# Kernel optimization log

Hardware: AMD Instinct MI355X
Metric: run time of the kernel (lower is better)

Reference implementation:

```python
import jax, jax.numpy as jnp
import numpy as np

B, N, K, Q = 2, 4096, 48, 20  # batch, nodes, neighbors, Potts states (amino acids)


def setup_inputs() -> dict:
    key = jax.random.key(0)
    k1, k2, k3, k4 = jax.random.split(key, 4)
    h = jax.random.normal(k1, (B, N, Q), dtype=jnp.float32)
    J = jax.random.normal(k2, (B, N, K, Q, Q), dtype=jnp.float32)
    edge_idx = jax.random.randint(k3, (B, N, K), 0, N)
    S = jax.random.randint(k4, (B, N), 0, Q)
    return {"S": S, "h": h, "J": J, "edge_idx": edge_idx}


def reference(S, h, J, edge_idx):
    """Potts energy: U (B,), U_i (B,N,Q). Faithful to compute_potts_energy."""
    Bs, Ns, Ks, Qs, _ = J.shape
    # collect_neighbors: S_j[b,i,k] = S[b, edge_idx[b,i,k]]
    S_j = jnp.take_along_axis(S, edge_idx.reshape(Bs, Ns * Ks), axis=1).reshape(Bs, Ns, Ks)
    # J_ij[b,i,k,q] = J[b,i,k,q, S_j[b,i,k]]  (gather along last state axis)
    idx = jnp.broadcast_to(S_j[..., None, None], (Bs, Ns, Ks, Qs, 1))
    J_ij = jnp.take_along_axis(J, idx, axis=-1)[..., 0]      # (B,N,K,Q)
    J_i = J_ij.sum(axis=2)                                    # (B,N,Q)
    U_i = h + J_i
    gather_s = lambda T: jnp.take_along_axis(T, S[..., None], axis=-1)[..., 0]  # (B,N)
    U = (gather_s(U_i) - 0.5 * gather_s(J_i)).sum(axis=1)     # (B,)
    return U, U_i
```

## Files before the change

kernel.cpp:

```cpp
#include <hip/hip_runtime.h>


constexpr int Bc = 2;
constexpr int Nc = 4096;
constexpr int Kc = 48;
constexpr int Qc = 20;
constexpr int NODE_FLOATS = Kc * Qc * Qc;

__global__ __launch_bounds__(64) void potts_gather_kernel(
    const int*   __restrict__ S,
    const float* __restrict__ h,
    const float* __restrict__ J,
    const int*   __restrict__ edge_idx,
    float*       __restrict__ U_i_out,
    float*       __restrict__ node_c)
{
    const int node = blockIdx.x;
    const int b    = node >> 12;
    const int l    = threadIdx.x;

    __shared__ float T[Kc][Qc + 1];

    const int s_i = S[node];

    if (l < Kc) {
        const int e  = edge_idx[node * Kc + l];
        const int sl = S[b * Nc + e];
        const float* Jp = J + (size_t)node * NODE_FLOATS + l * (Qc * Qc) + sl;
        float v[Qc];
        #pragma unroll
        for (int q = 0; q < Qc; ++q) v[q] = Jp[q * Qc];
        #pragma unroll
        for (int q = 0; q < Qc; ++q) T[l][q] = v[q];
    }
    __syncthreads();

    if (l < Qc) {
        float ji = 0.0f;
        #pragma unroll
        for (int k = 0; k < Kc; ++k) ji += T[k][l];
        const float ui = h[node * Qc + l] + ji;
        U_i_out[node * Qc + l] = ui;
        if (l == s_i) {
            node_c[node] = ui - 0.5f * ji;
        }
    }
}

__global__ __launch_bounds__(256) void potts_reduce_kernel(
    const float* __restrict__ node_c, float* __restrict__ U)
{
    const int b   = blockIdx.x;
    const int tid = threadIdx.x;
    float s = 0.0f;
    for (int i = tid; i < Nc; i += 256) s += node_c[b * Nc + i];
    #pragma unroll
    for (int off = 32; off > 0; off >>= 1) s += __shfl_down(s, off, 64);
    __shared__ float ws[4];
    if ((tid & 63) == 0) ws[tid >> 6] = s;
    __syncthreads();
    if (tid == 0) U[b] = ws[0] + ws[1] + ws[2] + ws[3];
}

extern "C" void kernel_launch(void* const* d_in, const int* in_sizes, int n_in,
                              void* d_out, int out_size, void* d_ws, size_t ws_size,
                              hipStream_t stream) {
    const int*   S        = (const int*)  d_in[0];
    const float* h        = (const float*)d_in[1];
    const float* J        = (const float*)d_in[2];
    const int*   edge_idx = (const int*)  d_in[3];

    float* out    = (float*)d_out;
    float* U      = out;
    float* U_i    = out + Bc;
    float* node_c = (float*)d_ws;

    potts_gather_kernel<<<Bc * Nc, 64, 0, stream>>>(S, h, J, edge_idx, U_i, node_c);
    potts_reduce_kernel<<<Bc, 256, 0, stream>>>(node_c, U);
}
```

Baseline: 796.1 us.

## Replace strided J gather with full coalesced float4 sweep and staged reduction

Splits the work into stages: precompute neighbor states Sj, then stream all of J with coalesced float4 loads, keeping only the selected column element into a workspace w2, then sum per node. The old kernel's strided scalar loads each touched a separate cache line, so DRAM traffic was dominated by sector over-fetch. The new plan reads all of J contiguously (about 302MB) instead of gathering about 15MB, and adds extra kernel launches plus w2 workspace traffic.

```diff
diff --git a/kernel.cpp b/kernel.cpp
--- a/kernel.cpp
+++ b/kernel.cpp
@@ -5,45 +5,66 @@
 constexpr int Nc = 4096;
 constexpr int Kc = 48;
 constexpr int Qc = 20;
-constexpr int NODE_FLOATS = Kc * Qc * Qc;
+constexpr int NODES   = Bc * Nc;
+constexpr int NODE_F4 = Kc * Qc * Qc / 4;
+constexpr long long TOT_F4 = (long long)NODES * NODE_F4;
+constexpr int SWEEP_BLOCKS = 2048;
+constexpr int SWEEP_TPB    = 256;
+constexpr int G     = SWEEP_BLOCKS * SWEEP_TPB;
+constexpr int ITERS = (int)(TOT_F4 / G);
 
-__global__ __launch_bounds__(64) void potts_gather_kernel(
-    const int*   __restrict__ S,
-    const float* __restrict__ h,
-    const float* __restrict__ J,
-    const int*   __restrict__ edge_idx,
-    float*       __restrict__ U_i_out,
+constexpr size_t WS_SJ = 0;
+constexpr size_t WS_NC = 512 * 1024;
+constexpr size_t WS_W2 = 1024 * 1024;
+
+__global__ __launch_bounds__(256) void sj_gather_kernel(
+    const int* __restrict__ S, const int* __restrict__ edge_idx,
+    int* __restrict__ Sj)
+{
+    const int g = blockIdx.x * 256 + threadIdx.x;
+    const int e = edge_idx[g];
+    const int b = (g >= Nc * Kc) ? 1 : 0;
+    Sj[g] = S[b * Nc + e];
+}
+
+__global__ __launch_bounds__(SWEEP_TPB, 8) void sweep_kernel(
+    const float* __restrict__ J, const int* __restrict__ Sj,
+    float* __restrict__ w2)
+{
+    const int g0 = blockIdx.x * SWEEP_TPB + threadIdx.x;
+    const float4* Jf = (const float4*)J;
+    #pragma unroll 5
+    for (int i = 0; i < ITERS; ++i) {
+        const int m = g0 + i * G;
+        float4 v = Jf[m];
+        int mk = m / 100;
+        int r  = m - mk * 100;
+        int q  = r / 5;
+        int s0 = (r - q * 5) << 2;
+        int d  = Sj[mk] - s0;
+        if ((unsigned)d < 4u) {
+            float val = (d == 0) ? v.x : (d == 1) ? v.y : (d == 2) ? v.z : v.w;
+            w2[mk * 20 + q] = val;
+        }
+    }
+}
+
+__global__ __launch_bounds__(64) void node_sum_kernel(
+    const float* __restrict__ w2, const float* __restrict__ h,
+    const int*   __restrict__ S,  float* __restrict__ U_i_out,
     float*       __restrict__ node_c)
 {
     const int node = blockIdx.x;
-    const int b    = node >> 12;
     const int l    = threadIdx.x;
-
-    __shared__ float T[Kc][Qc + 1];
-
-    const int s_i = S[node];
-
-    if (l < Kc) {
-        const int e  = edge_idx[node * Kc + l];
-        const int sl = S[b * Nc + e];
-        const float* Jp = J + (size_t)node * NODE_FLOATS + l * (Qc * Qc) + sl;
-        float v[Qc];
-        #pragma unroll
-        for (int q = 0; q < Qc; ++q) v[q] = Jp[q * Qc];
-        #pragma unroll
-        for (int q = 0; q < Qc; ++q) T[l][q] = v[q];
-    }
-    __syncthreads();
-
+    const int s_i  = S[node];
     if (l < Qc) {
+        const float* p = w2 + (size_t)node * (Kc * Qc) + l;
         float ji = 0.0f;
         #pragma unroll
-        for (int k = 0; k < Kc; ++k) ji += T[k][l];
+        for (int k = 0; k < Kc; ++k) ji += p[k * Qc];
         const float ui = h[node * Qc + l] + ji;
         U_i_out[node * Qc + l] = ui;
-        if (l == s_i) {
-            node_c[node] = ui - 0.5f * ji;
-        }
+        if (l == s_i) node_c[node] = ui - 0.5f * ji;
     }
 }
 
@@ -73,8 +94,14 @@
     float* out    = (float*)d_out;
     float* U      = out;
     float* U_i    = out + Bc;
-    float* node_c = (float*)d_ws;
 
-    potts_gather_kernel<<<Bc * Nc, 64, 0, stream>>>(S, h, J, edge_idx, U_i, node_c);
+    float* wsf    = (float*)d_ws;
+    int*   Sj     = (int*)  (wsf + WS_SJ);
+    float* node_c =          wsf + WS_NC;
+    float* w2     =          wsf + WS_W2;
+
+    sj_gather_kernel<<<Bc * Nc * Kc / 256, 256, 0, stream>>>(S, edge_idx, Sj);
+    sweep_kernel<<<SWEEP_BLOCKS, SWEEP_TPB, 0, stream>>>(J, Sj, w2);
+    node_sum_kernel<<<NODES, 64, 0, stream>>>(w2, h, S, U_i, node_c);
     potts_reduce_kernel<<<Bc, 256, 0, stream>>>(node_c, U);
 }
```

After: 816.1 us. 2.5% more time.
